# Kernel tuning notes

Hardware: AMD Instinct MI355X
Metric: run time of the kernel (lower is better)

## Reference

```python
import jax, jax.numpy as jnp
import numpy as np

N, E, D, L, G, C = 20000, 320000, 512, 6, 64, 10
EPS = 1e-5


def setup_inputs() -> dict:
    key = jax.random.key(0)
    ks = jax.random.split(key, 8)
    s = 0.05  # small init scale to keep activations sane across 6 layers
    x = jax.random.normal(ks[0], (N, D), jnp.float32)
    edge_index = jax.random.randint(ks[1], (2, E), 0, N, jnp.int32)
    batch = jnp.sort(jax.random.randint(ks[2], (N,), 0, G, jnp.int32))
    W_rel = jax.random.normal(ks[3], (L, D, D), jnp.float32) * s
    b_rel = jnp.zeros((L, D), jnp.float32)
    W_root = jax.random.normal(ks[4], (L, D, D), jnp.float32) * s
    gamma = jnp.ones((L, D), jnp.float32)
    beta = jnp.zeros((L, D), jnp.float32)
    lin_w = jax.random.normal(ks[5], (D, C), jnp.float32) * s
    lin_b = jnp.zeros((C,), jnp.float32)
    return {"x": x, "edge_index": edge_index, "batch": batch,
            "W_rel": W_rel, "b_rel": b_rel, "W_root": W_root,
            "gamma": gamma, "beta": beta, "lin_w": lin_w, "lin_b": lin_b}


def reference(x, edge_index, batch, W_rel, b_rel, W_root, gamma, beta, lin_w, lin_b):
    # PyG GraphConv (aggr='add'): out = segment_sum(x[src] -> dst) @ W_rel + b_rel + x @ W_root
    src, dst = edge_index[0], edge_index[1]
    n = x.shape[0]
    for l in range(W_rel.shape[0]):  # 6 structurally identical layers
        agg = jax.ops.segment_sum(x[src], dst, num_segments=n)  # [N, D]
        h = agg @ W_rel[l] + b_rel[l] + x @ W_root[l]
        # BatchNorm1d in training mode: biased batch statistics over nodes
        mu = jnp.mean(h, axis=0)
        var = jnp.mean(jnp.square(h - mu), axis=0)
        x = jax.nn.relu((h - mu) * jax.lax.rsqrt(var + EPS) * gamma[l] + beta[l])
    # global_mean_pool over per-node graph ids
    sums = jax.ops.segment_sum(x, batch, num_segments=G)              # [G, D]
    counts = jax.ops.segment_sum(jnp.ones((n,), x.dtype), batch, num_segments=G)
    pooled = sums / jnp.maximum(counts, 1.0)[:, None]
    return pooled @ lin_w + lin_b  # [G, C]
```

## Files before the change

kernel.cpp:

```cpp
#include <hip/hip_runtime.h>


typedef unsigned short u16;
typedef unsigned int u32;
typedef __attribute__((ext_vector_type(8))) short bf16x8;
typedef __attribute__((ext_vector_type(16))) float f32x16;

#define DFEAT 512
#define KDIM 1024
#define NLAYER 6
#define NGRAPH 64
#define NCLS 10
#define BN_EPS 1e-5f

__device__ __forceinline__ float bf_lo(u32 u) { union { u32 i; float f; } v; v.i = u << 16; return v.f; }
__device__ __forceinline__ float bf_hi(u32 u) { union { u32 i; float f; } v; v.i = u & 0xFFFF0000u; return v.f; }
__device__ __forceinline__ u16 f2bf(float f) {
  union { float f; u32 i; } v; v.f = f;
  u32 r = v.i + 0x7FFFu + ((v.i >> 16) & 1u);
  return (u16)(r >> 16);
}
__device__ __forceinline__ u32 pack2(float lo, float hi) {
  return (u32)f2bf(lo) | ((u32)f2bf(hi) << 16);
}

__device__ __forceinline__ void gload_lds16(const u16* g, u16* lds_base) {
  __builtin_amdgcn_global_load_lds(
      (const __attribute__((address_space(1))) u32*)g,
      (__attribute__((address_space(3))) u32*)lds_base, 16, 0, 0);
}

__global__ void prep_kernel(const int* __restrict__ ei, int* __restrict__ counts, int E,
                            const float* __restrict__ Wrel, const float* __restrict__ Wroot,
                            u16* __restrict__ Wt,
                            const float* __restrict__ x, u16* __restrict__ A, int M,
                            int histB, int wB) {
  __shared__ float tile[64][65];
  int b = blockIdx.x;
  int tid = threadIdx.x;
  if (b < histB) {
    int e = b * 256 + tid;
    if (e < E) atomicAdd(&counts[ei[E + e]], 1);
  } else if (b < histB + wB) {
    int t = b - histB;
    int l = t >> 7;
    int tt = t & 127;
    int k0 = (tt >> 3) << 6;
    int n0 = (tt & 7) << 6;
    int rr = tid >> 4;
    int c4 = (tid & 15) << 2;
#pragma unroll
    for (int i = 0; i < 4; i++) {
      int k = k0 + i * 16 + rr;
      const float* src = (k < DFEAT)
          ? &Wrel[((size_t)l * DFEAT + k) * DFEAT + n0 + c4]
          : &Wroot[((size_t)l * DFEAT + (k - DFEAT)) * DFEAT + n0 + c4];
      float4 v = *(const float4*)src;
      float* d = &tile[i * 16 + rr][c4];
      d[0] = v.x; d[1] = v.y; d[2] = v.z; d[3] = v.w;
    }
    __syncthreads();
    int nr = tid >> 3;
    int kc = (tid & 7) << 3;
#pragma unroll
    for (int i = 0; i < 2; i++) {
      int nl = i * 32 + nr;
      uint4 o;
      o.x = pack2(tile[kc + 0][nl], tile[kc + 1][nl]);
      o.y = pack2(tile[kc + 2][nl], tile[kc + 3][nl]);
      o.z = pack2(tile[kc + 4][nl], tile[kc + 5][nl]);
      o.w = pack2(tile[kc + 6][nl], tile[kc + 7][nl]);
      *(uint4*)&Wt[(size_t)(l * DFEAT + n0 + nl) * KDIM + k0 + kc] = o;
    }
  } else {
    int idx = (b - histB - wB) * 256 + tid;
    int row = idx >> 7;
    int c4 = (idx & 127) * 4;
    if (row < M) {
      float4 v = *(const float4*)&x[(size_t)row * DFEAT + c4];
      uint2 o; o.x = pack2(v.x, v.y); o.y = pack2(v.z, v.w);
      *(uint2*)&A[(size_t)row * KDIM + DFEAT + c4] = o;
    }
  }
}

#define SCHUNK 20
__global__ __launch_bounds__(1024) void scan_kernel(const int* __restrict__ counts,
                                                    int* __restrict__ row_ptr,
                                                    int* __restrict__ cursor, int n) {
  __shared__ int part[1024];
  int tid = threadIdx.x;
  int base = tid * SCHUNK;
  int loc[SCHUNK];
  int s = 0;
#pragma unroll
  for (int i = 0; i < SCHUNK; i++) {
    int idx = base + i;
    int v = (idx < n) ? counts[idx] : 0;
    loc[i] = s; s += v;
  }
  part[tid] = s;
  __syncthreads();
  int x = s;
  for (int off = 1; off < 1024; off <<= 1) {
    int t = (tid >= off) ? part[tid - off] : 0;
    __syncthreads();
    x += t;
    part[tid] = x;
    __syncthreads();
  }
  int offset = x - s;
#pragma unroll
  for (int i = 0; i < SCHUNK; i++) {
    int idx = base + i;
    if (idx < n) { int v = offset + loc[i]; row_ptr[idx] = v; cursor[idx] = v; }
  }
  if (tid == 1023) row_ptr[n] = offset + s;
}

__global__ void scatter_kernel(const int* __restrict__ ei, int* __restrict__ cursor,
                               int* __restrict__ csr_src, int E) {
  int e = blockIdx.x * 256 + threadIdx.x;
  if (e < E) {
    int d = ei[E + e];
    int pos = atomicAdd(&cursor[d], 1);
    csr_src[pos] = ei[e];
  }
}

template <bool FUSED>
__device__ __forceinline__ void acc8(uint4 v, const float* sc, const float* sh, float2* a) {
  if constexpr (FUSED) {
    a[0].x += fmaxf(bf_lo(v.x) * sc[0] + sh[0], 0.f);
    a[0].y += fmaxf(bf_hi(v.x) * sc[1] + sh[1], 0.f);
    a[1].x += fmaxf(bf_lo(v.y) * sc[2] + sh[2], 0.f);
    a[1].y += fmaxf(bf_hi(v.y) * sc[3] + sh[3], 0.f);
    a[2].x += fmaxf(bf_lo(v.z) * sc[4] + sh[4], 0.f);
    a[2].y += fmaxf(bf_hi(v.z) * sc[5] + sh[5], 0.f);
    a[3].x += fmaxf(bf_lo(v.w) * sc[6] + sh[6], 0.f);
    a[3].y += fmaxf(bf_hi(v.w) * sc[7] + sh[7], 0.f);
  } else {
    a[0] += make_float2(bf_lo(v.x), bf_hi(v.x));
    a[1] += make_float2(bf_lo(v.y), bf_hi(v.y));
    a[2] += make_float2(bf_lo(v.z), bf_hi(v.z));
    a[3] += make_float2(bf_lo(v.w), bf_hi(v.w));
  }
}

#define GCAP 1536
template <bool FUSED>
__global__ __launch_bounds__(256) void gather_kernel(u16* __restrict__ A,
                                                     const u16* __restrict__ Hb,
                                                     const float* __restrict__ sums,
                                                     const float* __restrict__ gamma,
                                                     const float* __restrict__ beta,
                                                     const int* __restrict__ row_ptr,
                                                     const int* __restrict__ csr_src,
                                                     int n, float invN) {
  __shared__ int sidx[GCAP];
  int b = blockIdx.x;
  int slice = b & 7;
  int grp = b >> 3;
  int tid = threadIdx.x;
  int r0 = grp * 32;
  int rend = (r0 + 32 < n) ? (r0 + 32) : n;
  int wbeg = row_ptr[r0], wend = row_ptr[rend];
  int cnt = wend - wbeg;
  bool lds_ok = (cnt <= GCAP);
  if (lds_ok)
    for (int t = tid; t < cnt; t += 256) sidx[t] = csr_src[wbeg + t];
  __syncthreads();

  int wid = tid >> 6, lane = tid & 63;
  int dsub = lane >> 3, fl = lane & 7;
  int dst = r0 + wid * 8 + dsub;
  if (dst >= n) return;
  int cc = slice * 64 + fl * 8;
  float sc[8], sh[8];
  if constexpr (FUSED) {
#pragma unroll
    for (int j = 0; j < 8; j++) {
      int c = cc + j;
      float mu = sums[c] * invN;
      float var = sums[DFEAT + c] * invN - mu * mu;
      float s = gamma[c] * rsqrtf(var + BN_EPS);
      sc[j] = s;
      sh[j] = beta[c] - mu * s;
    }
    uint4 h = *(const uint4*)&Hb[(size_t)dst * DFEAT + cc];
    uint4 o;
    o.x = pack2(fmaxf(bf_lo(h.x) * sc[0] + sh[0], 0.f), fmaxf(bf_hi(h.x) * sc[1] + sh[1], 0.f));
    o.y = pack2(fmaxf(bf_lo(h.y) * sc[2] + sh[2], 0.f), fmaxf(bf_hi(h.y) * sc[3] + sh[3], 0.f));
    o.z = pack2(fmaxf(bf_lo(h.z) * sc[4] + sh[4], 0.f), fmaxf(bf_hi(h.z) * sc[5] + sh[5], 0.f));
    o.w = pack2(fmaxf(bf_lo(h.w) * sc[6] + sh[6], 0.f), fmaxf(bf_hi(h.w) * sc[7] + sh[7], 0.f));
    *(uint4*)&A[(size_t)dst * KDIM + DFEAT + cc] = o;
  }
  const u16* Sx = FUSED ? (Hb + cc) : (A + DFEAT + cc);
  const size_t RS = FUSED ? DFEAT : KDIM;
  int db = row_ptr[dst], de = row_ptr[dst + 1];
  float2 a[4] = {};
  if (lds_ok) {
    int e = db - wbeg, ee = de - wbeg;
    for (; e + 7 < ee; e += 8) {
      int s0 = sidx[e + 0], s1 = sidx[e + 1], s2 = sidx[e + 2], s3 = sidx[e + 3];
      int s4 = sidx[e + 4], s5 = sidx[e + 5], s6 = sidx[e + 6], s7 = sidx[e + 7];
      uint4 v0 = *(const uint4*)&Sx[(size_t)s0 * RS];
      uint4 v1 = *(const uint4*)&Sx[(size_t)s1 * RS];
      uint4 v2 = *(const uint4*)&Sx[(size_t)s2 * RS];
      uint4 v3 = *(const uint4*)&Sx[(size_t)s3 * RS];
      uint4 v4 = *(const uint4*)&Sx[(size_t)s4 * RS];
      uint4 v5 = *(const uint4*)&Sx[(size_t)s5 * RS];
      uint4 v6 = *(const uint4*)&Sx[(size_t)s6 * RS];
      uint4 v7 = *(const uint4*)&Sx[(size_t)s7 * RS];
      acc8<FUSED>(v0, sc, sh, a); acc8<FUSED>(v1, sc, sh, a);
      acc8<FUSED>(v2, sc, sh, a); acc8<FUSED>(v3, sc, sh, a);
      acc8<FUSED>(v4, sc, sh, a); acc8<FUSED>(v5, sc, sh, a);
      acc8<FUSED>(v6, sc, sh, a); acc8<FUSED>(v7, sc, sh, a);
    }
    for (; e < ee; ++e) {
      uint4 v = *(const uint4*)&Sx[(size_t)sidx[e] * RS];
      acc8<FUSED>(v, sc, sh, a);
    }
  } else {
    for (int e = db; e < de; ++e) {
      uint4 v = *(const uint4*)&Sx[(size_t)csr_src[e] * RS];
      acc8<FUSED>(v, sc, sh, a);
    }
  }
  uint4 o;
  o.x = pack2(a[0].x, a[0].y); o.y = pack2(a[1].x, a[1].y);
  o.z = pack2(a[2].x, a[2].y); o.w = pack2(a[3].x, a[3].y);
  *(uint4*)&A[(size_t)dst * KDIM + cc] = o;
}

#define BM 128
#define BN 128
#define BK 64
#define CSTR 132
__global__ __launch_bounds__(256, 4) void gemm_kernel(const u16* __restrict__ A,
                                                      const u16* __restrict__ Bt,
                                                      const float* __restrict__ bias,
                                                      u16* __restrict__ Hb,
                                                      float* __restrict__ sums, int M) {
  const int lin = blockIdx.x;
  const int bx = ((lin >> 5) << 3) + (lin & 7);
  const int by = (lin >> 3) & 3;
  const int m0 = bx * BM;
  if (m0 >= M) return;
  const int n0 = by * BN;

  __shared__ u16 smem[BM * CSTR];
  __shared__ float sred[2 * BN];
  u16* As = smem;
  u16* Bs = smem + BM * BK;
  const int tid = threadIdx.x;
  const int wid = tid >> 6, lane = tid & 63;
  const int wm = wid >> 1, wn = wid & 1;
  const int l31 = lane & 31, half = lane >> 5;

  if (tid < 2 * BN) sred[tid] = 0.f;

  const int dr = lane >> 3;
  const int gcol = ((lane & 7) ^ dr) * 8;
  int arow[4], brow[4];
#pragma unroll
  for (int t = 0; t < 4; t++) {
    int r = wid * 32 + t * 8 + dr;
    int ar = m0 + r; if (ar >= M) ar = M - 1;
    arow[t] = ar;
    brow[t] = n0 + r;
  }

  f32x16 acc[2][2] = {};

  for (int k0 = 0; k0 < KDIM; k0 += BK) {
    __syncthreads();
#pragma unroll
    for (int t = 0; t < 4; t++)
      gload_lds16(&A[(size_t)arow[t] * KDIM + k0 + gcol], &As[(wid * 32 + t * 8) * BK]);
#pragma unroll
    for (int t = 0; t < 4; t++)
      gload_lds16(&Bt[(size_t)brow[t] * KDIM + k0 + gcol], &Bs[(wid * 32 + t * 8) * BK]);
    __syncthreads();
#pragma unroll
    for (int ks = 0; ks < 4; ks++) {
      int slot = ((ks * 2 + half) ^ (l31 & 7)) * 8;
      bf16x8 a0 = *(const bf16x8*)&As[(wm * 64 + l31) * BK + slot];
      bf16x8 a1 = *(const bf16x8*)&As[(wm * 64 + 32 + l31) * BK + slot];
      bf16x8 b0 = *(const bf16x8*)&Bs[(wn * 64 + l31) * BK + slot];
      bf16x8 b1 = *(const bf16x8*)&Bs[(wn * 64 + 32 + l31) * BK + slot];
      acc[0][0] = __builtin_amdgcn_mfma_f32_32x32x16_bf16(a0, b0, acc[0][0], 0, 0, 0);
      acc[0][1] = __builtin_amdgcn_mfma_f32_32x32x16_bf16(a0, b1, acc[0][1], 0, 0, 0);
      acc[1][0] = __builtin_amdgcn_mfma_f32_32x32x16_bf16(a1, b0, acc[1][0], 0, 0, 0);
      acc[1][1] = __builtin_amdgcn_mfma_f32_32x32x16_bf16(a1, b1, acc[1][1], 0, 0, 0);
    }
  }

  __syncthreads();

#pragma unroll
  for (int nt = 0; nt < 2; nt++) {
    int colt = wn * 64 + nt * 32 + l31;
    float bv = bias[n0 + colt];
    float s = 0.f, s2 = 0.f;
#pragma unroll
    for (int mt = 0; mt < 2; mt++) {
      int rbase = wm * 64 + mt * 32 + half * 4;
#pragma unroll
      for (int reg = 0; reg < 16; reg++) {
        int rowt = rbase + (reg & 3) + 8 * (reg >> 2);
        float v = acc[mt][nt][reg] + bv;
        smem[rowt * CSTR + colt] = f2bf(v);
        if (m0 + rowt < M) { s += v; s2 += v * v; }
      }
    }
    s  += __shfl_xor(s, 32);
    s2 += __shfl_xor(s2, 32);
    if (half == 0) {
      atomicAdd(&sred[colt], s);
      atomicAdd(&sred[BN + colt], s2);
    }
  }
  __syncthreads();

  const int rsub = tid >> 4;
  const int c8 = (tid & 15) * 8;
#pragma unroll
  for (int it = 0; it < 8; it++) {
    int rowt = it * 16 + rsub;
    int grow = m0 + rowt;
    if (grow < M) {
      uint4 v = *(const uint4*)&smem[rowt * CSTR + c8];
      *(uint4*)&Hb[(size_t)grow * DFEAT + n0 + c8] = v;
    }
  }
  if (tid < BN) {
    atomicAdd(&sums[n0 + tid], sred[tid]);
    atomicAdd(&sums[DFEAT + n0 + tid], sred[BN + tid]);
  }
}

__device__ __forceinline__ int lower_bound_dev(const int* a, int n, int v) {
  int lo = 0, hi = n;
  while (lo < hi) { int mid = (lo + hi) >> 1; if (a[mid] < v) lo = mid + 1; else hi = mid; }
  return lo;
}

__global__ __launch_bounds__(1024) void pool_kernel(const u16* __restrict__ Hb,
                                                    const float* __restrict__ sums,
                                                    const float* __restrict__ gamma,
                                                    const float* __restrict__ beta,
                                                    const int* __restrict__ batch,
                                                    float* __restrict__ pooled, int n, float invN) {
  __shared__ float red[DFEAT];
  int g = blockIdx.x;
  int tid = threadIdx.x;
  if (tid < DFEAT) red[tid] = 0.f;
  int lo = lower_bound_dev(batch, n, g);
  int hi = lower_bound_dev(batch, n, g + 1);
  int rowOff = tid >> 6, lane = tid & 63;
  int c0 = lane * 8;
  float sc[8], sh[8];
#pragma unroll
  for (int j = 0; j < 8; j++) {
    int c = c0 + j;
    float mu = sums[c] * invN;
    float var = sums[DFEAT + c] * invN - mu * mu;
    float s = gamma[c] * rsqrtf(var + BN_EPS);
    sc[j] = s;
    sh[j] = beta[c] - mu * s;
  }
  float a[8] = {};
  for (int r = lo + rowOff; r < hi; r += 16) {
    uint4 v = *(const uint4*)&Hb[(size_t)r * DFEAT + c0];
    float e0 = bf_lo(v.x), e1 = bf_hi(v.x), e2 = bf_lo(v.y), e3 = bf_hi(v.y);
    float e4 = bf_lo(v.z), e5 = bf_hi(v.z), e6 = bf_lo(v.w), e7 = bf_hi(v.w);
    a[0] += fmaxf(e0 * sc[0] + sh[0], 0.f); a[1] += fmaxf(e1 * sc[1] + sh[1], 0.f);
    a[2] += fmaxf(e2 * sc[2] + sh[2], 0.f); a[3] += fmaxf(e3 * sc[3] + sh[3], 0.f);
    a[4] += fmaxf(e4 * sc[4] + sh[4], 0.f); a[5] += fmaxf(e5 * sc[5] + sh[5], 0.f);
    a[6] += fmaxf(e6 * sc[6] + sh[6], 0.f); a[7] += fmaxf(e7 * sc[7] + sh[7], 0.f);
  }
  __syncthreads();
#pragma unroll
  for (int j = 0; j < 8; j++) atomicAdd(&red[c0 + j], a[j]);
  __syncthreads();
  if (tid < DFEAT) pooled[g * DFEAT + tid] = red[tid] / fmaxf((float)(hi - lo), 1.0f);
}

__global__ __launch_bounds__(64) void final_kernel(const float* __restrict__ pooled,
                                                   const float* __restrict__ lin_w,
                                                   const float* __restrict__ lin_b,
                                                   float* __restrict__ out) {
  int g = blockIdx.x;
  int lane = threadIdx.x;
  float acc[NCLS] = {};
  float4 p0 = *(const float4*)&pooled[g * DFEAT + lane * 8];
  float4 p1 = *(const float4*)&pooled[g * DFEAT + lane * 8 + 4];
  float pv[8] = {p0.x, p0.y, p0.z, p0.w, p1.x, p1.y, p1.z, p1.w};
#pragma unroll
  for (int j = 0; j < 8; j++) {
    int k = lane * 8 + j;
#pragma unroll
    for (int c = 0; c < NCLS; c++) acc[c] += pv[j] * lin_w[k * NCLS + c];
  }
#pragma unroll
  for (int off = 32; off > 0; off >>= 1)
#pragma unroll
    for (int c = 0; c < NCLS; c++) acc[c] += __shfl_down(acc[c], off);
  if (lane == 0)
#pragma unroll
    for (int c = 0; c < NCLS; c++) out[g * NCLS + c] = acc[c] + lin_b[c];
}

extern "C" void kernel_launch(void* const* d_in, const int* in_sizes, int n_in,
                              void* d_out, int out_size, void* d_ws, size_t ws_size,
                              hipStream_t stream) {
  const float* x      = (const float*)d_in[0];
  const int*   ei     = (const int*)d_in[1];
  const int*   batch  = (const int*)d_in[2];
  const float* W_rel  = (const float*)d_in[3];
  const float* b_rel  = (const float*)d_in[4];
  const float* W_root = (const float*)d_in[5];
  const float* gamma  = (const float*)d_in[6];
  const float* beta   = (const float*)d_in[7];
  const float* lin_w  = (const float*)d_in[8];
  const float* lin_b  = (const float*)d_in[9];
  float* out = (float*)d_out;

  const int N = in_sizes[0] / DFEAT;
  const int E = in_sizes[1] / 2;

  char* p = (char*)d_ws;
  u16*   A       = (u16*)p;    p += (size_t)N * KDIM * 2;
  u16*   Hb      = (u16*)p;    p += (size_t)N * DFEAT * 2;
  u16*   Wt      = (u16*)p;    p += (size_t)NLAYER * DFEAT * KDIM * 2;
  int*   row_ptr = (int*)p;    p += ((size_t)(N + 1) * 4 + 15) / 16 * 16;
  int*   cursor  = (int*)p;    p += (size_t)N * 4;
  int*   csr_src = (int*)p;    p += (size_t)E * 4;
  float* sums    = (float*)p;  p += (size_t)NLAYER * 2 * DFEAT * 4;
  float* pooled  = (float*)p;  p += (size_t)NGRAPH * DFEAT * 4;

  const float invN = 1.0f / (float)N;

  hipMemsetAsync(cursor, 0, (size_t)N * 4, stream);
  hipMemsetAsync(sums, 0, (size_t)NLAYER * 2 * DFEAT * 4, stream);

  const int histB = (E + 255) / 256;
  const int wB = NLAYER * 128;
  const int xB = (N * 128 + 255) / 256;
  prep_kernel<<<histB + wB + xB, 256, 0, stream>>>(ei, cursor, E, W_rel, W_root, Wt,
                                                   x, A, N, histB, wB);
  scan_kernel<<<1, 1024, 0, stream>>>(cursor, row_ptr, cursor, N);
  scatter_kernel<<<(E + 255) / 256, 256, 0, stream>>>(ei, cursor, csr_src, E);

  const int ngrp8 = ((N + 31) / 32) * 8;
  const int gtiles = (((N + BM - 1) / BM + 7) / 8) * 8 * 4;

  for (int l = 0; l < NLAYER; ++l) {
    float* sums_l = sums + (size_t)l * 2 * DFEAT;
    if (l == 0)
      gather_kernel<false><<<ngrp8, 256, 0, stream>>>(A, Hb, nullptr, nullptr, nullptr,
                                                      row_ptr, csr_src, N, invN);
    else
      gather_kernel<true><<<ngrp8, 256, 0, stream>>>(A, Hb,
          sums + (size_t)(l - 1) * 2 * DFEAT,
          gamma + (size_t)(l - 1) * DFEAT, beta + (size_t)(l - 1) * DFEAT,
          row_ptr, csr_src, N, invN);
    gemm_kernel<<<gtiles, 256, 0, stream>>>(A, Wt + (size_t)l * DFEAT * KDIM,
                                            b_rel + (size_t)l * DFEAT, Hb, sums_l, N);
  }

  pool_kernel<<<NGRAPH, 1024, 0, stream>>>(Hb, sums + (size_t)(NLAYER - 1) * 2 * DFEAT,
                                           gamma + (size_t)(NLAYER - 1) * DFEAT,
                                           beta + (size_t)(NLAYER - 1) * DFEAT,
                                           batch, pooled, N, invN);
  final_kernel<<<NGRAPH, 64, 0, stream>>>(pooled, lin_w, lin_b, out);
}
```

Baseline: 625.1 us.

## Sort destination nodes by in-degree to balance gather warps

Builds a degree-bucketed permutation of destination nodes: a degree histogram and scans produce per-bucket bases, and a rank kernel assigns each node a slot so that neighbouring rows in the CSR have equal degree. The gather kernel then walks nodes in that permuted order, so the eight rows sharing a wavefront have matching edge counts and lanes diverge less. The accumulate and BN-ReLU math is also rewritten with 2-wide float vectors so the compiler can emit packed FMA and max. This adds an extra kernel launch and an indirection through perm, loses locality of destination writes, and caps bucket degree at 1023, which would break CSR offsets for higher-degree nodes.

```diff
diff --git a/kernel.cpp b/kernel.cpp
--- a/kernel.cpp
+++ b/kernel.cpp
@@ -5,6 +5,7 @@
 typedef unsigned int u32;
 typedef __attribute__((ext_vector_type(8))) short bf16x8;
 typedef __attribute__((ext_vector_type(16))) float f32x16;
+typedef __attribute__((ext_vector_type(2))) float f32x2;
 
 #define DFEAT 512
 #define KDIM 1024
@@ -12,6 +13,7 @@
 #define NGRAPH 64
 #define NCLS 10
 #define BN_EPS 1e-5f
+#define NBUCKET 1024
 
 __device__ __forceinline__ float bf_lo(u32 u) { union { u32 i; float f; } v; v.i = u << 16; return v.f; }
 __device__ __forceinline__ float bf_hi(u32 u) { union { u32 i; float f; } v; v.i = u & 0xFFFF0000u; return v.f; }
@@ -84,66 +86,104 @@
   }
 }
 
-#define SCHUNK 20
-__global__ __launch_bounds__(1024) void scan_kernel(const int* __restrict__ counts,
-                                                    int* __restrict__ row_ptr,
-                                                    int* __restrict__ cursor, int n) {
-  __shared__ int part[1024];
+__global__ __launch_bounds__(1024) void dscan_kernel(const int* __restrict__ counts,
+                                                     int* __restrict__ base0,
+                                                     int* __restrict__ bcur,
+                                                     int* __restrict__ edgebase,
+                                                     int* __restrict__ row_ptr2, int n) {
+  __shared__ int hist[NBUCKET];
+  __shared__ int part[NBUCKET];
   int tid = threadIdx.x;
-  int base = tid * SCHUNK;
-  int loc[SCHUNK];
-  int s = 0;
-#pragma unroll
-  for (int i = 0; i < SCHUNK; i++) {
-    int idx = base + i;
-    int v = (idx < n) ? counts[idx] : 0;
-    loc[i] = s; s += v;
-  }
-  part[tid] = s;
-  __syncthreads();
-  int x = s;
-  for (int off = 1; off < 1024; off <<= 1) {
+  hist[tid] = 0;
+  __syncthreads();
+  for (int i = tid; i < n; i += 1024) {
+    int d = counts[i]; if (d > NBUCKET - 1) d = NBUCKET - 1;
+    atomicAdd(&hist[d], 1);
+  }
+  __syncthreads();
+  int c = hist[tid];
+  part[tid] = c; __syncthreads();
+  int x = c;
+  for (int off = 1; off < NBUCKET; off <<= 1) {
     int t = (tid >= off) ? part[tid - off] : 0;
     __syncthreads();
-    x += t;
-    part[tid] = x;
-    __syncthreads();
-  }
-  int offset = x - s;
-#pragma unroll
-  for (int i = 0; i < SCHUNK; i++) {
-    int idx = base + i;
-    if (idx < n) { int v = offset + loc[i]; row_ptr[idx] = v; cursor[idx] = v; }
-  }
-  if (tid == 1023) row_ptr[n] = offset + s;
-}
-
-__global__ void scatter_kernel(const int* __restrict__ ei, int* __restrict__ cursor,
-                               int* __restrict__ csr_src, int E) {
+    x += t; part[tid] = x;
+    __syncthreads();
+  }
+  base0[tid] = x - c;
+  bcur[tid] = x - c;
+  int w = c * tid;
+  part[tid] = w; __syncthreads();
+  int y = w;
+  for (int off = 1; off < NBUCKET; off <<= 1) {
+    int t = (tid >= off) ? part[tid - off] : 0;
+    __syncthreads();
+    y += t; part[tid] = y;
+    __syncthreads();
+  }
+  edgebase[tid] = y - w;
+  if (tid == NBUCKET - 1) row_ptr2[n] = y;
+}
+
+__global__ __launch_bounds__(256) void rank_kernel(const int* __restrict__ counts,
+                                                   const int* __restrict__ base0,
+                                                   int* __restrict__ bcur,
+                                                   const int* __restrict__ edgebase,
+                                                   int* __restrict__ perm,
+                                                   int* __restrict__ row_ptr2,
+                                                   int* __restrict__ cursor2, int n) {
+  __shared__ int hb[NBUCKET];
+  __shared__ int hstart[NBUCKET];
+  int tid = threadIdx.x;
+  for (int d = tid; d < NBUCKET; d += 256) hb[d] = 0;
+  __syncthreads();
+  int row = blockIdx.x * 256 + tid;
+  bool valid = (row < n);
+  int deg = 0, j = 0;
+  if (valid) {
+    deg = counts[row]; if (deg > NBUCKET - 1) deg = NBUCKET - 1;
+    j = atomicAdd(&hb[deg], 1);
+  }
+  __syncthreads();
+  for (int d = tid; d < NBUCKET; d += 256) {
+    int c = hb[d];
+    hstart[d] = c ? atomicAdd(&bcur[d], c) : 0;
+  }
+  __syncthreads();
+  if (valid) {
+    int rnk = hstart[deg] + j;
+    int jj = rnk - base0[deg];
+    int v = edgebase[deg] + jj * deg;
+    perm[rnk] = row;
+    row_ptr2[rnk] = v;
+    cursor2[row] = v;
+  }
+}
+
+__global__ void scatter_kernel(const int* __restrict__ ei, int* __restrict__ cursor2,
+                               int* __restrict__ csr2, int E) {
   int e = blockIdx.x * 256 + threadIdx.x;
   if (e < E) {
     int d = ei[E + e];
-    int pos = atomicAdd(&cursor[d], 1);
-    csr_src[pos] = ei[e];
+    int pos = atomicAdd(&cursor2[d], 1);
+    csr2[pos] = ei[e];
   }
 }
 
 template <bool FUSED>
-__device__ __forceinline__ void acc8(uint4 v, const float* sc, const float* sh, float2* a) {
+__device__ __forceinline__ void acc8(uint4 v, const f32x2* sc, const f32x2* sh, f32x2* a) {
+  f32x2 t0 = {bf_lo(v.x), bf_hi(v.x)};
+  f32x2 t1 = {bf_lo(v.y), bf_hi(v.y)};
+  f32x2 t2 = {bf_lo(v.z), bf_hi(v.z)};
+  f32x2 t3 = {bf_lo(v.w), bf_hi(v.w)};
   if constexpr (FUSED) {
-    a[0].x += fmaxf(bf_lo(v.x) * sc[0] + sh[0], 0.f);
-    a[0].y += fmaxf(bf_hi(v.x) * sc[1] + sh[1], 0.f);
-    a[1].x += fmaxf(bf_lo(v.y) * sc[2] + sh[2], 0.f);
-    a[1].y += fmaxf(bf_hi(v.y) * sc[3] + sh[3], 0.f);
-    a[2].x += fmaxf(bf_lo(v.z) * sc[4] + sh[4], 0.f);
-    a[2].y += fmaxf(bf_hi(v.z) * sc[5] + sh[5], 0.f);
-    a[3].x += fmaxf(bf_lo(v.w) * sc[6] + sh[6], 0.f);
-    a[3].y += fmaxf(bf_hi(v.w) * sc[7] + sh[7], 0.f);
+    f32x2 z = {0.f, 0.f};
+    a[0] += __builtin_elementwise_max(t0 * sc[0] + sh[0], z);
+    a[1] += __builtin_elementwise_max(t1 * sc[1] + sh[1], z);
+    a[2] += __builtin_elementwise_max(t2 * sc[2] + sh[2], z);
+    a[3] += __builtin_elementwise_max(t3 * sc[3] + sh[3], z);
   } else {
-    a[0] += make_float2(bf_lo(v.x), bf_hi(v.x));
-    a[1] += make_float2(bf_lo(v.y), bf_hi(v.y));
-    a[2] += make_float2(bf_lo(v.z), bf_hi(v.z));
-    a[3] += make_float2(bf_lo(v.w), bf_hi(v.w));
+    a[0] += t0; a[1] += t1; a[2] += t2; a[3] += t3;
   }
 }
 
@@ -154,8 +194,9 @@
                                                      const float* __restrict__ sums,
                                                      const float* __restrict__ gamma,
                                                      const float* __restrict__ beta,
-                                                     const int* __restrict__ row_ptr,
-                                                     const int* __restrict__ csr_src,
+                                                     const int* __restrict__ row_ptr2,
+                                                     const int* __restrict__ csr2,
+                                                     const int* __restrict__ perm,
                                                      int n, float invN) {
   __shared__ int sidx[GCAP];
   int b = blockIdx.x;
@@ -164,19 +205,20 @@
   int tid = threadIdx.x;
   int r0 = grp * 32;
   int rend = (r0 + 32 < n) ? (r0 + 32) : n;
-  int wbeg = row_ptr[r0], wend = row_ptr[rend];
+  int wbeg = row_ptr2[r0], wend = row_ptr2[rend];
   int cnt = wend - wbeg;
   bool lds_ok = (cnt <= GCAP);
   if (lds_ok)
-    for (int t = tid; t < cnt; t += 256) sidx[t] = csr_src[wbeg + t];
+    for (int t = tid; t < cnt; t += 256) sidx[t] = csr2[wbeg + t];
   __syncthreads();
 
   int wid = tid >> 6, lane = tid & 63;
   int dsub = lane >> 3, fl = lane & 7;
-  int dst = r0 + wid * 8 + dsub;
-  if (dst >= n) return;
+  int rnk = r0 + wid * 8 + dsub;
+  if (rnk >= n) return;
+  int dst = perm[rnk];
   int cc = slice * 64 + fl * 8;
-  float sc[8], sh[8];
+  f32x2 sc2[4], sh2[4];
   if constexpr (FUSED) {
 #pragma unroll
     for (int j = 0; j < 8; j++) {
@@ -184,21 +226,24 @@
       float mu = sums[c] * invN;
       float var = sums[DFEAT + c] * invN - mu * mu;
       float s = gamma[c] * rsqrtf(var + BN_EPS);
-      sc[j] = s;
-      sh[j] = beta[c] - mu * s;
+      sc2[j >> 1][j & 1] = s;
+      sh2[j >> 1][j & 1] = beta[c] - mu * s;
     }
     uint4 h = *(const uint4*)&Hb[(size_t)dst * DFEAT + cc];
+    f32x2 z = {0.f, 0.f};
+    f32x2 e0 = __builtin_elementwise_max((f32x2){bf_lo(h.x), bf_hi(h.x)} * sc2[0] + sh2[0], z);
+    f32x2 e1 = __builtin_elementwise_max((f32x2){bf_lo(h.y), bf_hi(h.y)} * sc2[1] + sh2[1], z);
+    f32x2 e2 = __builtin_elementwise_max((f32x2){bf_lo(h.z), bf_hi(h.z)} * sc2[2] + sh2[2], z);
+    f32x2 e3 = __builtin_elementwise_max((f32x2){bf_lo(h.w), bf_hi(h.w)} * sc2[3] + sh2[3], z);
     uint4 o;
-    o.x = pack2(fmaxf(bf_lo(h.x) * sc[0] + sh[0], 0.f), fmaxf(bf_hi(h.x) * sc[1] + sh[1], 0.f));
-    o.y = pack2(fmaxf(bf_lo(h.y) * sc[2] + sh[2], 0.f), fmaxf(bf_hi(h.y) * sc[3] + sh[3], 0.f));
-    o.z = pack2(fmaxf(bf_lo(h.z) * sc[4] + sh[4], 0.f), fmaxf(bf_hi(h.z) * sc[5] + sh[5], 0.f));
-    o.w = pack2(fmaxf(bf_lo(h.w) * sc[6] + sh[6], 0.f), fmaxf(bf_hi(h.w) * sc[7] + sh[7], 0.f));
+    o.x = pack2(e0[0], e0[1]); o.y = pack2(e1[0], e1[1]);
+    o.z = pack2(e2[0], e2[1]); o.w = pack2(e3[0], e3[1]);
     *(uint4*)&A[(size_t)dst * KDIM + DFEAT + cc] = o;
   }
   const u16* Sx = FUSED ? (Hb + cc) : (A + DFEAT + cc);
   const size_t RS = FUSED ? DFEAT : KDIM;
-  int db = row_ptr[dst], de = row_ptr[dst + 1];
-  float2 a[4] = {};
+  int db = row_ptr2[rnk], de = row_ptr2[rnk + 1];
+  f32x2 a[4] = {};
   if (lds_ok) {
     int e = db - wbeg, ee = de - wbeg;
     for (; e + 7 < ee; e += 8) {
@@ -212,24 +257,24 @@
       uint4 v5 = *(const uint4*)&Sx[(size_t)s5 * RS];
       uint4 v6 = *(const uint4*)&Sx[(size_t)s6 * RS];
       uint4 v7 = *(const uint4*)&Sx[(size_t)s7 * RS];
-      acc8<FUSED>(v0, sc, sh, a); acc8<FUSED>(v1, sc, sh, a);
-      acc8<FUSED>(v2, sc, sh, a); acc8<FUSED>(v3, sc, sh, a);
-      acc8<FUSED>(v4, sc, sh, a); acc8<FUSED>(v5, sc, sh, a);
-      acc8<FUSED>(v6, sc, sh, a); acc8<FUSED>(v7, sc, sh, a);
+      acc8<FUSED>(v0, sc2, sh2, a); acc8<FUSED>(v1, sc2, sh2, a);
+      acc8<FUSED>(v2, sc2, sh2, a); acc8<FUSED>(v3, sc2, sh2, a);
+      acc8<FUSED>(v4, sc2, sh2, a); acc8<FUSED>(v5, sc2, sh2, a);
+      acc8<FUSED>(v6, sc2, sh2, a); acc8<FUSED>(v7, sc2, sh2, a);
     }
     for (; e < ee; ++e) {
       uint4 v = *(const uint4*)&Sx[(size_t)sidx[e] * RS];
-      acc8<FUSED>(v, sc, sh, a);
+      acc8<FUSED>(v, sc2, sh2, a);
     }
   } else {
     for (int e = db; e < de; ++e) {
-      uint4 v = *(const uint4*)&Sx[(size_t)csr_src[e] * RS];
-      acc8<FUSED>(v, sc, sh, a);
+      uint4 v = *(const uint4*)&Sx[(size_t)csr2[e] * RS];
+      acc8<FUSED>(v, sc2, sh2, a);
     }
   }
   uint4 o;
-  o.x = pack2(a[0].x, a[0].y); o.y = pack2(a[1].x, a[1].y);
-  o.z = pack2(a[2].x, a[2].y); o.w = pack2(a[3].x, a[3].y);
+  o.x = pack2(a[0][0], a[0][1]); o.y = pack2(a[1][0], a[1][1]);
+  o.z = pack2(a[2][0], a[2][1]); o.w = pack2(a[3][0], a[3][1]);
   *(uint4*)&A[(size_t)dst * KDIM + cc] = o;
 }
 
@@ -431,27 +476,34 @@
   const int E = in_sizes[1] / 2;
 
   char* p = (char*)d_ws;
-  u16*   A       = (u16*)p;    p += (size_t)N * KDIM * 2;
-  u16*   Hb      = (u16*)p;    p += (size_t)N * DFEAT * 2;
-  u16*   Wt      = (u16*)p;    p += (size_t)NLAYER * DFEAT * KDIM * 2;
-  int*   row_ptr = (int*)p;    p += ((size_t)(N + 1) * 4 + 15) / 16 * 16;
-  int*   cursor  = (int*)p;    p += (size_t)N * 4;
-  int*   csr_src = (int*)p;    p += (size_t)E * 4;
-  float* sums    = (float*)p;  p += (size_t)NLAYER * 2 * DFEAT * 4;
-  float* pooled  = (float*)p;  p += (size_t)NGRAPH * DFEAT * 4;
+  u16*   A        = (u16*)p;    p += (size_t)N * KDIM * 2;
+  u16*   Hb       = (u16*)p;    p += (size_t)N * DFEAT * 2;
+  u16*   Wt       = (u16*)p;    p += (size_t)NLAYER * DFEAT * KDIM * 2;
+  int*   row_ptr2 = (int*)p;    p += ((size_t)(N + 1) * 4 + 15) / 16 * 16;
+  int*   counts   = (int*)p;    p += (size_t)N * 4;
+  int*   cursor2  = (int*)p;    p += (size_t)N * 4;
+  int*   perm     = (int*)p;    p += (size_t)N * 4;
+  int*   csr2     = (int*)p;    p += (size_t)E * 4;
+  int*   base0    = (int*)p;    p += (size_t)NBUCKET * 4;
+  int*   bcur     = (int*)p;    p += (size_t)NBUCKET * 4;
+  int*   edgebase = (int*)p;    p += (size_t)NBUCKET * 4;
+  float* sums     = (float*)p;  p += (size_t)NLAYER * 2 * DFEAT * 4;
+  float* pooled   = (float*)p;  p += (size_t)NGRAPH * DFEAT * 4;
 
   const float invN = 1.0f / (float)N;
 
-  hipMemsetAsync(cursor, 0, (size_t)N * 4, stream);
+  hipMemsetAsync(counts, 0, (size_t)N * 4, stream);
   hipMemsetAsync(sums, 0, (size_t)NLAYER * 2 * DFEAT * 4, stream);
 
   const int histB = (E + 255) / 256;
   const int wB = NLAYER * 128;
   const int xB = (N * 128 + 255) / 256;
-  prep_kernel<<<histB + wB + xB, 256, 0, stream>>>(ei, cursor, E, W_rel, W_root, Wt,
+  prep_kernel<<<histB + wB + xB, 256, 0, stream>>>(ei, counts, E, W_rel, W_root, Wt,
                                                    x, A, N, histB, wB);
-  scan_kernel<<<1, 1024, 0, stream>>>(cursor, row_ptr, cursor, N);
-  scatter_kernel<<<(E + 255) / 256, 256, 0, stream>>>(ei, cursor, csr_src, E);
+  dscan_kernel<<<1, 1024, 0, stream>>>(counts, base0, bcur, edgebase, row_ptr2, N);
+  rank_kernel<<<(N + 255) / 256, 256, 0, stream>>>(counts, base0, bcur, edgebase,
+                                                   perm, row_ptr2, cursor2, N);
+  scatter_kernel<<<(E + 255) / 256, 256, 0, stream>>>(ei, cursor2, csr2, E);
 
   const int ngrp8 = ((N + 31) / 32) * 8;
   const int gtiles = (((N + BM - 1) / BM + 7) / 8) * 8 * 4;
@@ -460,12 +512,12 @@
     float* sums_l = sums + (size_t)l * 2 * DFEAT;
     if (l == 0)
       gather_kernel<false><<<ngrp8, 256, 0, stream>>>(A, Hb, nullptr, nullptr, nullptr,
-                                                      row_ptr, csr_src, N, invN);
+                                                      row_ptr2, csr2, perm, N, invN);
     else
       gather_kernel<true><<<ngrp8, 256, 0, stream>>>(A, Hb,
           sums + (size_t)(l - 1) * 2 * DFEAT,
           gamma + (size_t)(l - 1) * DFEAT, beta + (size_t)(l - 1) * DFEAT,
-          row_ptr, csr_src, N, invN);
+          row_ptr2, csr2, perm, N, invN);
     gemm_kernel<<<gtiles, 256, 0, stream>>>(A, Wt + (size_t)l * DFEAT * KDIM,
                                             b_rel + (size_t)l * DFEAT, Hb, sums_l, N);
   }
```

Measured after the change: 562.3 us. 1.11x faster.
